# Kernel tuning notes

Measured on AMD Instinct MI355X. Metric: run time of the kernel, lower is better.

## Reference

```python
import jax, jax.numpy as jnp
import numpy as np

N_S = 50000
N_T = 50000
E = 800000
D_IN = 128
D_OUT = 128


def setup_inputs() -> dict:
    key = jax.random.key(0)
    k1, k2, k3, k4 = jax.random.split(key, 4)
    edge_index = jax.random.randint(k1, (2, E), 0, N_S, dtype=jnp.int64)
    x_s = jax.random.normal(k2, (N_S, D_IN), dtype=jnp.float32)
    x_t = jax.random.normal(k3, (N_T, D_IN), dtype=jnp.float32)
    # glorot-ish linear weight of GCNConv (bias=False)
    W = jax.random.normal(k4, (D_IN, D_OUT), dtype=jnp.float32) * (1.0 / np.sqrt(D_IN))
    return {"edge_index": edge_index, "x_s": x_s, "x_t": x_t, "W": W}


def reference(edge_index, x_s, x_t, W):
    N_s = x_s.shape[0]
    N_t = x_t.shape[0]
    N = N_s + N_t
    # dropout p=0.0 -> identity; concat bipartite features
    x = jnp.concatenate([x_s, x_t], axis=0)  # [N, d_in]
    row = edge_index[0]
    col = edge_index[1] + N_s  # module shifts target indices in-place
    # GCNConv: add self-loops with weight 1
    loops = jnp.arange(N, dtype=row.dtype)
    row_f = jnp.concatenate([row, loops])
    col_f = jnp.concatenate([col, loops])
    w = jnp.ones(row_f.shape[0], dtype=x.dtype)
    # symmetric degree normalization: deg computed on target (col)
    deg = jax.ops.segment_sum(w, col_f, num_segments=N)
    deg_inv_sqrt = jnp.where(deg > 0, jax.lax.rsqrt(deg), 0.0)
    norm = deg_inv_sqrt[row_f] * deg_inv_sqrt[col_f]  # [E+N]
    # linear transform then normalized scatter-add aggregation
    h = x @ W  # [N, d_out]
    msg = h[row_f] * norm[:, None]  # gather + scale, [E+N, d_out]
    out = jax.ops.segment_sum(msg, col_f, num_segments=N)  # scatter-add
    out = jax.nn.relu(out)
    return out[:N_s], out[N_s:]
```

## Files before the change

kernel.cpp:

```cpp
#include <hip/hip_runtime.h>
#include <hip/hip_bf16.h>
#include <math.h>

#define NSRC 50000
#define NTGT 50000
#define NTOT 100000
#define NEDGE 800000
#define DIM 128

#define NBUCK 782
#define BCAP 1536
#define BPAD 16
#define BLK 512
#define EPT 4
#define EPB 2048
#define PBLK 391
#define GEMM_GRID 782

typedef __attribute__((ext_vector_type(8))) short short8;
typedef __attribute__((ext_vector_type(4))) float float4v;

union U8 { short8 s; uint4 u; };

__device__ __forceinline__ unsigned short f2bf(float f) {
    unsigned u = __float_as_uint(f);
    unsigned r = (u + 0x7FFFu + ((u >> 16) & 1u)) >> 16;
    return (unsigned short)r;
}
__device__ __forceinline__ float bf2f(unsigned us) {
    return __uint_as_float(us << 16);
}
__device__ __forceinline__ unsigned pkbf(float lo, float hi) {
    __hip_bfloat162 b = __float22bfloat162_rn(make_float2(lo, hi));
    return *(unsigned*)&b;
}

__global__ __launch_bounds__(256) void k_prep(const float* __restrict__ W,
                                              unsigned short* __restrict__ Wt,
                                              int* __restrict__ bcnt) {
    int i = blockIdx.x * 256 + threadIdx.x;
    if (i < NBUCK * BPAD) bcnt[i] = 0;
    int j = i & 7, lane = (i >> 3) & 63, ts = i >> 9;
    int t = ts >> 2, s = ts & 3;
    int nl = lane & 15, qd = lane >> 4;
    Wt[i] = f2bf(W[(s * 32 + qd * 8 + j) * DIM + (t * 16 + nl)]);
}

__global__ __launch_bounds__(BLK) void k_part(const int* __restrict__ row,
                                              const int* __restrict__ col,
                                              int* __restrict__ bcnt,
                                              unsigned* __restrict__ part) {
    __shared__ int hist[NBUCK], runbase[NBUCK], cur[NBUCK];
    int tid = threadIdx.x;
    for (int i = tid; i < NBUCK; i += BLK) hist[i] = 0;
    __syncthreads();

    int e0 = blockIdx.x * EPB + tid * EPT;
    bool valid = (e0 + EPT <= NEDGE);
    int c[EPT], r[EPT];
    if (valid) {
        *(int4*)&c[0] = *(const int4*)(col + e0);
        *(int4*)&r[0] = *(const int4*)(row + e0);
#pragma unroll
        for (int i = 0; i < EPT; ++i) atomicAdd(&hist[c[i] >> 6], 1);
    }
    __syncthreads();
    for (int i = tid; i < NBUCK; i += BLK) {
        runbase[i] = atomicAdd(&bcnt[i * BPAD], hist[i]);
        cur[i] = 0;
    }
    __syncthreads();
    if (valid) {
#pragma unroll
        for (int i = 0; i < EPT; ++i) {
            int q = c[i] >> 6;
            int pos = runbase[q] + atomicAdd(&cur[q], 1);
            part[q * BCAP + pos] = (unsigned)r[i] | ((unsigned)(c[i] & 63) << 16);
        }
    }
}

__global__ __launch_bounds__(BLK) void k_gemm(const float* __restrict__ xsrc,
                                              const float* __restrict__ xtgt,
                                              const unsigned short* __restrict__ Wt,
                                              unsigned short* __restrict__ h,
                                              float* __restrict__ out) {
    __shared__ unsigned short Bs[DIM * DIM];

    const int tid = threadIdx.x;
    for (int idx = tid; idx < 2048; idx += BLK)
        ((uint4*)Bs)[idx] = ((const uint4*)Wt)[idx];

    const int wave = tid >> 6, lane = tid & 63;
    const int nl = lane & 15, quad = lane >> 4;

    int node = blockIdx.x * 128 + wave * 16 + nl;
    int mc = (node < NTOT) ? node : (NTOT - 1);
    const float* xrow = (mc < NSRC) ? (xsrc + (size_t)mc * DIM)
                                    : (xtgt + (size_t)(mc - NSRC) * DIM);
    float4 a[8];
#pragma unroll
    for (int s = 0; s < 4; ++s) {
        a[2 * s]     = *(const float4*)(xrow + s * 32 + quad * 8);
        a[2 * s + 1] = *(const float4*)(xrow + s * 32 + quad * 8 + 4);
    }
    __syncthreads();

    float4v acc[8];
#pragma unroll
    for (int t = 0; t < 8; ++t) acc[t] = (float4v){0.f, 0.f, 0.f, 0.f};

#pragma unroll
    for (int s = 0; s < 4; ++s) {
        U8 af;
        af.u.x = pkbf(a[2 * s].x, a[2 * s].y);
        af.u.y = pkbf(a[2 * s].z, a[2 * s].w);
        af.u.z = pkbf(a[2 * s + 1].x, a[2 * s + 1].y);
        af.u.w = pkbf(a[2 * s + 1].z, a[2 * s + 1].w);
#pragma unroll
        for (int t = 0; t < 8; ++t) {
            short8 bf = *(const short8*)&Bs[((t * 4 + s) * 64 + lane) * 8];
            acc[t] = __builtin_amdgcn_mfma_f32_16x16x32_bf16(bf, af.s, acc[t], 0, 0, 0);
        }
    }

    if (node < NTOT) {
        unsigned short* hp = h + (size_t)node * DIM + quad * 4;
        float* op = out + (size_t)node * DIM + quad * 4;
        bool isrc = (node < NSRC);
#pragma unroll
        for (int t = 0; t < 8; ++t) {
            uint2 p;
            p.x = pkbf(acc[t][0], acc[t][1]);
            p.y = pkbf(acc[t][2], acc[t][3]);
            *(uint2*)(hp + t * 16) = p;
            if (isrc) {
                float4 o;
                o.x = fmaxf(acc[t][0], 0.f);
                o.y = fmaxf(acc[t][1], 0.f);
                o.z = fmaxf(acc[t][2], 0.f);
                o.w = fmaxf(acc[t][3], 0.f);
                *(float4*)(op + t * 16) = o;
            }
        }
    }
}

__global__ __launch_bounds__(BLK) void k_back(const int* __restrict__ bcnt,
                                              const unsigned* __restrict__ part,
                                              const unsigned short* __restrict__ h,
                                              float* __restrict__ out) {
    __shared__ unsigned short srt[BCAP];
    __shared__ int hist[256], st[256], cur[256], bufA[256], bufB[256];
    __shared__ int degs[64];

    int q = blockIdx.x, tid = threadIdx.x;
    int n = bcnt[q * BPAD];
    int base = q * BCAP;

    if (tid < 256) hist[tid] = 0;
    __syncthreads();
    for (int i = tid; i < n; i += BLK) {
        unsigned p = part[base + i];
        int key = (((p >> 14) & 3) << 6) | (p >> 16);
        atomicAdd(&hist[key], 1);
    }
    __syncthreads();
    if (tid < 64)
        degs[tid] = hist[tid] + hist[tid + 64] + hist[tid + 128] + hist[tid + 192];
    if (tid < 256) bufA[tid] = hist[tid];
    int* src = bufA; int* dst = bufB;
    for (int d = 1; d < 256; d <<= 1) {
        __syncthreads();
        if (tid < 256) dst[tid] = src[tid] + ((tid >= d) ? src[tid - d] : 0);
        int* tp = src; src = dst; dst = tp;
    }
    __syncthreads();
    if (tid < 256) { int e = src[tid] - hist[tid]; st[tid] = e; cur[tid] = e; }
    __syncthreads();
    for (int i = tid; i < n; i += BLK) {
        unsigned p = part[base + i];
        int key = (((p >> 14) & 3) << 6) | (p >> 16);
        int pos = atomicAdd(&cur[key], 1);
        srt[pos] = (unsigned short)(p & 0xffffu);
    }
    __syncthreads();

    int w = tid >> 6, lane = tid & 63;
    int qd = lane >> 4, ql = lane & 15;
    int cl0 = w * 8;

    float acc[8][8];
#pragma unroll
    for (int t = 0; t < 8; ++t)
#pragma unroll
        for (int j = 0; j < 8; ++j) acc[t][j] = 0.f;

#pragma unroll
    for (int p = 0; p < 4; ++p) {
#pragma unroll
        for (int t = 0; t < 8; ++t) {
            int seg = (p << 6) | (cl0 + t);
            int ns = hist[seg], s0 = st[seg];
            int kk = 0;
            for (; kk + 4 <= ns; kk += 4) {
                int r = (int)srt[s0 + kk + qd];
                uint4 d = *(const uint4*)(h + (size_t)r * DIM + ql * 8);
                acc[t][0] += bf2f(d.x & 0xffff); acc[t][1] += bf2f(d.x >> 16);
                acc[t][2] += bf2f(d.y & 0xffff); acc[t][3] += bf2f(d.y >> 16);
                acc[t][4] += bf2f(d.z & 0xffff); acc[t][5] += bf2f(d.z >> 16);
                acc[t][6] += bf2f(d.w & 0xffff); acc[t][7] += bf2f(d.w >> 16);
            }
            if (qd < ns - kk) {
                int r = (int)srt[s0 + kk + qd];
                uint4 d = *(const uint4*)(h + (size_t)r * DIM + ql * 8);
                acc[t][0] += bf2f(d.x & 0xffff); acc[t][1] += bf2f(d.x >> 16);
                acc[t][2] += bf2f(d.y & 0xffff); acc[t][3] += bf2f(d.y >> 16);
                acc[t][4] += bf2f(d.z & 0xffff); acc[t][5] += bf2f(d.z >> 16);
                acc[t][6] += bf2f(d.w & 0xffff); acc[t][7] += bf2f(d.w >> 16);
            }
        }
    }

#pragma unroll
    for (int t = 0; t < 8; ++t) {
#pragma unroll
        for (int j = 0; j < 8; ++j) {
            acc[t][j] += __shfl_xor(acc[t][j], 16, 64);
            acc[t][j] += __shfl_xor(acc[t][j], 32, 64);
        }
        int c = q * 64 + cl0 + t;
        if (qd == 0 && c < NTGT) {
            int nn = degs[cl0 + t];
            float di = rsqrtf(1.0f + (float)nn);
            float dd = di * di;
            uint4 dh = *(const uint4*)(h + (size_t)(NSRC + c) * DIM + ql * 8);
            float4 o0, o1;
            o0.x = fmaxf(di * acc[t][0] + dd * bf2f(dh.x & 0xffff), 0.f);
            o0.y = fmaxf(di * acc[t][1] + dd * bf2f(dh.x >> 16), 0.f);
            o0.z = fmaxf(di * acc[t][2] + dd * bf2f(dh.y & 0xffff), 0.f);
            o0.w = fmaxf(di * acc[t][3] + dd * bf2f(dh.y >> 16), 0.f);
            o1.x = fmaxf(di * acc[t][4] + dd * bf2f(dh.z & 0xffff), 0.f);
            o1.y = fmaxf(di * acc[t][5] + dd * bf2f(dh.z >> 16), 0.f);
            o1.z = fmaxf(di * acc[t][6] + dd * bf2f(dh.w & 0xffff), 0.f);
            o1.w = fmaxf(di * acc[t][7] + dd * bf2f(dh.w >> 16), 0.f);
            float* op = out + (size_t)(NSRC + c) * DIM + ql * 8;
            *(float4*)op = o0;
            *(float4*)(op + 4) = o1;
        }
    }
}

extern "C" void kernel_launch(void* const* d_in, const int* in_sizes, int n_in,
                              void* d_out, int out_size, void* d_ws, size_t ws_size,
                              hipStream_t stream) {
    const int* ei     = (const int*)d_in[0];
    const float* xsrc = (const float*)d_in[1];
    const float* xtgt = (const float*)d_in[2];
    const float* W    = (const float*)d_in[3];
    float* out = (float*)d_out;

    const int* row = ei;
    const int* col = ei + NEDGE;

    char* ws = (char*)d_ws;
    unsigned short* h  = (unsigned short*)ws;  ws += (size_t)NTOT * DIM * 2;
    unsigned short* Wt = (unsigned short*)ws;  ws += DIM * DIM * 2;
    unsigned* part = (unsigned*)ws;            ws += (size_t)NBUCK * BCAP * 4;
    int* bcnt = (int*)ws;                      ws += NBUCK * BPAD * 4;

    k_prep<<<64, 256, 0, stream>>>(W, Wt, bcnt);
    k_part<<<PBLK, BLK, 0, stream>>>(row, col, bcnt, part);
    k_gemm<<<GEMM_GRID, BLK, 0, stream>>>(xsrc, xtgt, Wt, h, out);
    k_back<<<NBUCK, BLK, 0, stream>>>(bcnt, part, h, out);
}
```

Measured before the change: 197.0 us.

## Halve target bucket size and restructure aggregation to interleave two targets per wave

Buckets now cover 32 target nodes instead of 64, which doubles the number of aggregation blocks and shrinks per-block shared state. Each wave now processes two targets at a time, interleaving their gathers to raise memory-level parallelism and cut register pressure (16 accumulators instead of 64). Bucket entries are cached in shared memory so the partition buffer is read once, and the old 4-way sub-sort is dropped. The risk is more blocks and more global atomics on bucket counters during partitioning, plus a higher chance that a smaller bucket overflows its capacity.

```diff
diff --git a/kernel.cpp b/kernel.cpp
--- a/kernel.cpp
+++ b/kernel.cpp
@@ -8,8 +8,8 @@
 #define NEDGE 800000
 #define DIM 128
 
-#define NBUCK 782
-#define BCAP 1536
+#define NBUCK 1563
+#define BCAP 768
 #define BPAD 16
 #define BLK 512
 #define EPT 4
@@ -40,10 +40,12 @@
                                               int* __restrict__ bcnt) {
     int i = blockIdx.x * 256 + threadIdx.x;
     if (i < NBUCK * BPAD) bcnt[i] = 0;
-    int j = i & 7, lane = (i >> 3) & 63, ts = i >> 9;
-    int t = ts >> 2, s = ts & 3;
-    int nl = lane & 15, qd = lane >> 4;
-    Wt[i] = f2bf(W[(s * 32 + qd * 8 + j) * DIM + (t * 16 + nl)]);
+    if (i < DIM * DIM) {
+        int j = i & 7, lane = (i >> 3) & 63, ts = i >> 9;
+        int t = ts >> 2, s = ts & 3;
+        int nl = lane & 15, qd = lane >> 4;
+        Wt[i] = f2bf(W[(s * 32 + qd * 8 + j) * DIM + (t * 16 + nl)]);
+    }
 }
 
 __global__ __launch_bounds__(BLK) void k_part(const int* __restrict__ row,
@@ -62,7 +64,7 @@
         *(int4*)&c[0] = *(const int4*)(col + e0);
         *(int4*)&r[0] = *(const int4*)(row + e0);
 #pragma unroll
-        for (int i = 0; i < EPT; ++i) atomicAdd(&hist[c[i] >> 6], 1);
+        for (int i = 0; i < EPT; ++i) atomicAdd(&hist[c[i] >> 5], 1);
     }
     __syncthreads();
     for (int i = tid; i < NBUCK; i += BLK) {
@@ -73,9 +75,9 @@
     if (valid) {
 #pragma unroll
         for (int i = 0; i < EPT; ++i) {
-            int q = c[i] >> 6;
+            int q = c[i] >> 5;
             int pos = runbase[q] + atomicAdd(&cur[q], 1);
-            part[q * BCAP + pos] = (unsigned)r[i] | ((unsigned)(c[i] & 63) << 16);
+            part[q * BCAP + pos] = (unsigned)r[i] | ((unsigned)(c[i] & 31) << 16);
         }
     }
 }
@@ -150,101 +152,116 @@
                                               const unsigned* __restrict__ part,
                                               const unsigned short* __restrict__ h,
                                               float* __restrict__ out) {
+    __shared__ unsigned ebuf[BCAP];
     __shared__ unsigned short srt[BCAP];
-    __shared__ int hist[256], st[256], cur[256], bufA[256], bufB[256];
-    __shared__ int degs[64];
+    __shared__ int hist[32], st[32], cur[32], bufA[32], bufB[32];
 
     int q = blockIdx.x, tid = threadIdx.x;
     int n = bcnt[q * BPAD];
     int base = q * BCAP;
 
-    if (tid < 256) hist[tid] = 0;
+    if (tid < 32) hist[tid] = 0;
     __syncthreads();
     for (int i = tid; i < n; i += BLK) {
         unsigned p = part[base + i];
-        int key = (((p >> 14) & 3) << 6) | (p >> 16);
-        atomicAdd(&hist[key], 1);
-    }
-    __syncthreads();
-    if (tid < 64)
-        degs[tid] = hist[tid] + hist[tid + 64] + hist[tid + 128] + hist[tid + 192];
-    if (tid < 256) bufA[tid] = hist[tid];
+        ebuf[i] = p;
+        atomicAdd(&hist[p >> 16], 1);
+    }
+    __syncthreads();
+
+    if (tid < 32) bufA[tid] = hist[tid];
     int* src = bufA; int* dst = bufB;
-    for (int d = 1; d < 256; d <<= 1) {
+    for (int d = 1; d < 32; d <<= 1) {
         __syncthreads();
-        if (tid < 256) dst[tid] = src[tid] + ((tid >= d) ? src[tid - d] : 0);
+        if (tid < 32) dst[tid] = src[tid] + ((tid >= d) ? src[tid - d] : 0);
         int* tp = src; src = dst; dst = tp;
     }
     __syncthreads();
-    if (tid < 256) { int e = src[tid] - hist[tid]; st[tid] = e; cur[tid] = e; }
+    if (tid < 32) { int e = src[tid] - hist[tid]; st[tid] = e; cur[tid] = e; }
     __syncthreads();
     for (int i = tid; i < n; i += BLK) {
-        unsigned p = part[base + i];
-        int key = (((p >> 14) & 3) << 6) | (p >> 16);
-        int pos = atomicAdd(&cur[key], 1);
+        unsigned p = ebuf[i];
+        int pos = atomicAdd(&cur[p >> 16], 1);
         srt[pos] = (unsigned short)(p & 0xffffu);
     }
     __syncthreads();
 
     int w = tid >> 6, lane = tid & 63;
     int qd = lane >> 4, ql = lane & 15;
-    int cl0 = w * 8;
-
-    float acc[8][8];
-#pragma unroll
-    for (int t = 0; t < 8; ++t)
-#pragma unroll
-        for (int j = 0; j < 8; ++j) acc[t][j] = 0.f;
-
-#pragma unroll
-    for (int p = 0; p < 4; ++p) {
-#pragma unroll
-        for (int t = 0; t < 8; ++t) {
-            int seg = (p << 6) | (cl0 + t);
-            int ns = hist[seg], s0 = st[seg];
-            int kk = 0;
-            for (; kk + 4 <= ns; kk += 4) {
-                int r = (int)srt[s0 + kk + qd];
+    int cl0 = w * 4;
+
+    for (int pr = 0; pr < 2; ++pr) {
+        int ca = cl0 + pr * 2, cb = ca + 1;
+        int nA = hist[ca], sA = st[ca];
+        int nB = hist[cb], sB = st[cb];
+
+        float accA[8], accB[8];
+#pragma unroll
+        for (int i = 0; i < 8; ++i) { accA[i] = 0.f; accB[i] = 0.f; }
+
+        int itA = (nA + 3) >> 2, itB = (nB + 3) >> 2;
+        int itn = (itA > itB) ? itA : itB;
+        for (int k = 0; k < itn; ++k) {
+            int e = 4 * k + qd;
+            if (e < nA) {
+                int r = (int)srt[sA + e];
                 uint4 d = *(const uint4*)(h + (size_t)r * DIM + ql * 8);
-                acc[t][0] += bf2f(d.x & 0xffff); acc[t][1] += bf2f(d.x >> 16);
-                acc[t][2] += bf2f(d.y & 0xffff); acc[t][3] += bf2f(d.y >> 16);
-                acc[t][4] += bf2f(d.z & 0xffff); acc[t][5] += bf2f(d.z >> 16);
-                acc[t][6] += bf2f(d.w & 0xffff); acc[t][7] += bf2f(d.w >> 16);
+                accA[0] += bf2f(d.x & 0xffff); accA[1] += bf2f(d.x >> 16);
+                accA[2] += bf2f(d.y & 0xffff); accA[3] += bf2f(d.y >> 16);
+                accA[4] += bf2f(d.z & 0xffff); accA[5] += bf2f(d.z >> 16);
+                accA[6] += bf2f(d.w & 0xffff); accA[7] += bf2f(d.w >> 16);
             }
-            if (qd < ns - kk) {
-                int r = (int)srt[s0 + kk + qd];
+            if (e < nB) {
+                int r = (int)srt[sB + e];
                 uint4 d = *(const uint4*)(h + (size_t)r * DIM + ql * 8);
-                acc[t][0] += bf2f(d.x & 0xffff); acc[t][1] += bf2f(d.x >> 16);
-                acc[t][2] += bf2f(d.y & 0xffff); acc[t][3] += bf2f(d.y >> 16);
-                acc[t][4] += bf2f(d.z & 0xffff); acc[t][5] += bf2f(d.z >> 16);
-                acc[t][6] += bf2f(d.w & 0xffff); acc[t][7] += bf2f(d.w >> 16);
+                accB[0] += bf2f(d.x & 0xffff); accB[1] += bf2f(d.x >> 16);
+                accB[2] += bf2f(d.y & 0xffff); accB[3] += bf2f(d.y >> 16);
+                accB[4] += bf2f(d.z & 0xffff); accB[5] += bf2f(d.z >> 16);
+                accB[6] += bf2f(d.w & 0xffff); accB[7] += bf2f(d.w >> 16);
             }
         }
-    }
-
-#pragma unroll
-    for (int t = 0; t < 8; ++t) {
-#pragma unroll
-        for (int j = 0; j < 8; ++j) {
-            acc[t][j] += __shfl_xor(acc[t][j], 16, 64);
-            acc[t][j] += __shfl_xor(acc[t][j], 32, 64);
-        }
-        int c = q * 64 + cl0 + t;
-        if (qd == 0 && c < NTGT) {
-            int nn = degs[cl0 + t];
-            float di = rsqrtf(1.0f + (float)nn);
+
+#pragma unroll
+        for (int i = 0; i < 8; ++i) {
+            accA[i] += __shfl_xor(accA[i], 16, 64);
+            accA[i] += __shfl_xor(accA[i], 32, 64);
+            accB[i] += __shfl_xor(accB[i], 16, 64);
+            accB[i] += __shfl_xor(accB[i], 32, 64);
+        }
+
+        int c0 = q * 32 + ca;
+        if (qd == 0 && c0 < NTGT) {
+            float di = rsqrtf(1.0f + (float)nA);
             float dd = di * di;
-            uint4 dh = *(const uint4*)(h + (size_t)(NSRC + c) * DIM + ql * 8);
+            uint4 dh = *(const uint4*)(h + (size_t)(NSRC + c0) * DIM + ql * 8);
             float4 o0, o1;
-            o0.x = fmaxf(di * acc[t][0] + dd * bf2f(dh.x & 0xffff), 0.f);
-            o0.y = fmaxf(di * acc[t][1] + dd * bf2f(dh.x >> 16), 0.f);
-            o0.z = fmaxf(di * acc[t][2] + dd * bf2f(dh.y & 0xffff), 0.f);
-            o0.w = fmaxf(di * acc[t][3] + dd * bf2f(dh.y >> 16), 0.f);
-            o1.x = fmaxf(di * acc[t][4] + dd * bf2f(dh.z & 0xffff), 0.f);
-            o1.y = fmaxf(di * acc[t][5] + dd * bf2f(dh.z >> 16), 0.f);
-            o1.z = fmaxf(di * acc[t][6] + dd * bf2f(dh.w & 0xffff), 0.f);
-            o1.w = fmaxf(di * acc[t][7] + dd * bf2f(dh.w >> 16), 0.f);
-            float* op = out + (size_t)(NSRC + c) * DIM + ql * 8;
+            o0.x = fmaxf(di * accA[0] + dd * bf2f(dh.x & 0xffff), 0.f);
+            o0.y = fmaxf(di * accA[1] + dd * bf2f(dh.x >> 16), 0.f);
+            o0.z = fmaxf(di * accA[2] + dd * bf2f(dh.y & 0xffff), 0.f);
+            o0.w = fmaxf(di * accA[3] + dd * bf2f(dh.y >> 16), 0.f);
+            o1.x = fmaxf(di * accA[4] + dd * bf2f(dh.z & 0xffff), 0.f);
+            o1.y = fmaxf(di * accA[5] + dd * bf2f(dh.z >> 16), 0.f);
+            o1.z = fmaxf(di * accA[6] + dd * bf2f(dh.w & 0xffff), 0.f);
+            o1.w = fmaxf(di * accA[7] + dd * bf2f(dh.w >> 16), 0.f);
+            float* op = out + (size_t)(NSRC + c0) * DIM + ql * 8;
+            *(float4*)op = o0;
+            *(float4*)(op + 4) = o1;
+        }
+        int c1 = q * 32 + cb;
+        if (qd == 0 && c1 < NTGT) {
+            float di = rsqrtf(1.0f + (float)nB);
+            float dd = di * di;
+            uint4 dh = *(const uint4*)(h + (size_t)(NSRC + c1) * DIM + ql * 8);
+            float4 o0, o1;
+            o0.x = fmaxf(di * accB[0] + dd * bf2f(dh.x & 0xffff), 0.f);
+            o0.y = fmaxf(di * accB[1] + dd * bf2f(dh.x >> 16), 0.f);
+            o0.z = fmaxf(di * accB[2] + dd * bf2f(dh.y & 0xffff), 0.f);
+            o0.w = fmaxf(di * accB[3] + dd * bf2f(dh.y >> 16), 0.f);
+            o1.x = fmaxf(di * accB[4] + dd * bf2f(dh.z & 0xffff), 0.f);
+            o1.y = fmaxf(di * accB[5] + dd * bf2f(dh.z >> 16), 0.f);
+            o1.z = fmaxf(di * accB[6] + dd * bf2f(dh.w & 0xffff), 0.f);
+            o1.w = fmaxf(di * accB[7] + dd * bf2f(dh.w >> 16), 0.f);
+            float* op = out + (size_t)(NSRC + c1) * DIM + ql * 8;
             *(float4*)op = o0;
             *(float4*)(op + 4) = o1;
         }
@@ -269,7 +286,7 @@
     unsigned* part = (unsigned*)ws;            ws += (size_t)NBUCK * BCAP * 4;
     int* bcnt = (int*)ws;                      ws += NBUCK * BPAD * 4;
 
-    k_prep<<<64, 256, 0, stream>>>(W, Wt, bcnt);
+    k_prep<<<98, 256, 0, stream>>>(W, Wt, bcnt);
     k_part<<<PBLK, BLK, 0, stream>>>(row, col, bcnt, part);
     k_gemm<<<GEMM_GRID, BLK, 0, stream>>>(xsrc, xtgt, Wt, h, out);
     k_back<<<NBUCK, BLK, 0, stream>>>(bcnt, part, h, out);
```

After: 185.7 us. -5.7%, faster.
